# Performance work log

Measured on AMD Instinct MI355X. Metric: run time of the kernel, lower is better.

Reference implementation:

```python
import jax, jax.numpy as jnp
import numpy as np

DIM = 768
NUM_HEADS = 12
HEAD_DIM = DIM // NUM_HEADS
SCALE = HEAD_DIM ** -0.5


def setup_inputs() -> dict:
    key = jax.random.key(0)
    ks = jax.random.split(key, 4)
    x = jax.random.normal(ks[0], (8, 1024, DIM), dtype=jnp.float32)
    # nn.Linear stores weight as [out, in]; we keep that convention.
    w_qkv = jax.random.normal(ks[1], (3 * DIM, DIM), dtype=jnp.float32) * (DIM ** -0.5)
    w_proj = jax.random.normal(ks[2], (DIM, DIM), dtype=jnp.float32) * (DIM ** -0.5)
    b_proj = jax.random.normal(ks[3], (DIM,), dtype=jnp.float32) * 0.02
    return {"x": x, "w_qkv": w_qkv, "w_proj": w_proj, "b_proj": b_proj}


def reference(x, w_qkv, w_proj, b_proj):
    B, N, C = x.shape
    H, D = NUM_HEADS, HEAD_DIM
    # qkv: [B, N, 3C] -> [3, B, H, N, D]
    qkv = jnp.einsum('bnc,oc->bno', x, w_qkv)
    qkv = qkv.reshape(B, N, 3, H, D).transpose(2, 0, 3, 1, 4)
    q, k, v = qkv[0] * SCALE, qkv[1], qkv[2]
    # attention scores [B, H, N, N]
    attn = jnp.einsum('bhnd,bhmd->bhnm', q, k)
    attn = jax.nn.softmax(attn, axis=-1)
    # weighted values -> [B, N, C]
    out = jnp.einsum('bhnm,bhmd->bhnd', attn, v)
    out = out.transpose(0, 2, 1, 3).reshape(B, N, C)
    # output projection
    return jnp.einsum('bnc,oc->bno', out, w_proj) + b_proj
```

## Files before the change

### kernel.cpp

```cpp
#include <hip/hip_runtime.h>
#include <hip/hip_bf16.h>
#include <math.h>


typedef unsigned short u16;
typedef __attribute__((ext_vector_type(8))) short bf16x8;
typedef __attribute__((ext_vector_type(4))) float f32x4;
typedef __attribute__((ext_vector_type(4))) unsigned int u32x4;

#define MFMA_BF16(a, b, c) __builtin_amdgcn_mfma_f32_16x16x32_bf16((a), (b), (c), 0, 0, 0)

static __device__ __forceinline__ void gld_lds16(const void* g, void* l) {
  __builtin_amdgcn_global_load_lds(
      (__attribute__((address_space(1))) void*)(g),
      (__attribute__((address_space(3))) void*)(l), 16, 0, 0);
}

static __device__ __forceinline__ u16 f2bf(float f) {
  __hip_bfloat16 h = __float2bfloat16(f);
  return *(u16*)&h;
}

static __device__ __forceinline__ float fast_exp2(float x) {
#if __has_builtin(__builtin_amdgcn_exp2f)
  return __builtin_amdgcn_exp2f(x);
#else
  return exp2f(x);
#endif
}

static __device__ __forceinline__ void conv4(const float* src, u16* dst, int i) {
  const float4 v = *(const float4*)(src + i);
  float f0 = v.x, f1 = v.y, f2 = v.z, f3 = v.w;
  if (!isfinite(f0)) f0 = 0.f;
  if (!isfinite(f1)) f1 = 0.f;
  if (!isfinite(f2)) f2 = 0.f;
  if (!isfinite(f3)) f3 = 0.f;
  ushort4 o;
  o.x = f2bf(f0); o.y = f2bf(f1); o.z = f2bf(f2); o.w = f2bf(f3);
  *(ushort4*)(dst + i) = o;
}

__global__ __launch_bounds__(256) void convert3_kernel(
    const float* __restrict__ x,  u16* __restrict__ xb,
    const float* __restrict__ wq, u16* __restrict__ wqb,
    const float* __restrict__ wp, u16* __restrict__ wpb)
{
  const int blk = blockIdx.x;
  if (blk < 6144)      conv4(x,  xb,  (blk * 256 + threadIdx.x) * 4);
  else if (blk < 7872) conv4(wq, wqb, ((blk - 6144) * 256 + threadIdx.x) * 4);
  else                 conv4(wp, wpb, ((blk - 7872) * 256 + threadIdx.x) * 4);
}

__device__ __forceinline__ void gemm_tile_768(
    const u16* __restrict__ A, const u16* __restrict__ B,
    int m0, int n0, u16* ldsA, u16* ldsB, f32x4 acc[4][4])
{
  const int tid  = threadIdx.x;
  const int lane = tid & 63;
  const int wave = tid >> 6;
  const int quad = lane >> 4;
  const int l16  = lane & 15;
  const int wm = wave >> 1, wn = wave & 1;

  const u16* gA[4]; const u16* gB[4]; int ldsoff[4];
#pragma unroll
  for (int it = 0; it < 4; ++it) {
    const int c   = it * 256 + tid;
    const int row = c >> 3;
    const int cc  = (c & 7) ^ (row & 7);
    gA[it] = A + (size_t)(m0 + row) * 768 + cc * 8;
    gB[it] = B + (size_t)(n0 + row) * 768 + cc * 8;
    ldsoff[it] = (it * 256 + wave * 64) * 8;
  }

  for (int kt = 0; kt < 12; ++kt) {
    __syncthreads();
#pragma unroll
    for (int it = 0; it < 4; ++it) {
      gld_lds16(gA[it] + kt * 64, ldsA + ldsoff[it]);
      gld_lds16(gB[it] + kt * 64, ldsB + ldsoff[it]);
    }
    __syncthreads();
#pragma unroll
    for (int kc = 0; kc < 2; ++kc) {
      bf16x8 av[4], bv[4];
#pragma unroll
      for (int i = 0; i < 4; ++i) {
        const int rowA = wm * 64 + i * 16 + l16;
        av[i] = *(const bf16x8*)(ldsA + rowA * 64 + (((kc * 4 + quad) ^ (rowA & 7)) * 8));
        const int rowB = wn * 64 + i * 16 + l16;
        bv[i] = *(const bf16x8*)(ldsB + rowB * 64 + (((kc * 4 + quad) ^ (rowB & 7)) * 8));
      }
#pragma unroll
      for (int i = 0; i < 4; ++i)
#pragma unroll
        for (int j = 0; j < 4; ++j)
          acc[i][j] = MFMA_BF16(av[i], bv[j], acc[i][j]);
    }
  }
}


__global__ __launch_bounds__(256, 4) void qkv_gemm_kernel(
    const u16* __restrict__ X, const u16* __restrict__ W,
    u16* __restrict__ Qb, u16* __restrict__ Kb, u16* __restrict__ Vt)
{
  __shared__ alignas(16) u16 lds[2 * 128 * 64];
  u16* ldsA = lds;
  u16* ldsB = lds + 128 * 64;

  const int id0 = blockIdx.y * 18 + blockIdx.x;
  const int swz = (id0 & 7) * 144 + (id0 >> 3);
  const int bx  = swz % 18, by = swz / 18;
  const int n0 = bx * 128;
  const int m0 = by * 128;
  f32x4 acc[4][4];
  const f32x4 zero = {0.f, 0.f, 0.f, 0.f};
#pragma unroll
  for (int i = 0; i < 4; ++i)
#pragma unroll
    for (int j = 0; j < 4; ++j) acc[i][j] = zero;

  gemm_tile_768(X, W, m0, n0, ldsA, ldsB, acc);

  const int tid = threadIdx.x, lane = tid & 63, wave = tid >> 6;
  const int quad = lane >> 4, l16 = lane & 15;
  const int wm = wave >> 1, wn = wave & 1;

  const int which = bx / 6;
  const bool isV = (which == 2);
  const float sc = (which == 0) ? 0.180336880f : 1.0f;
  u16* ep = lds;

  __syncthreads();
#pragma unroll
  for (int i = 0; i < 4; ++i)
#pragma unroll
    for (int j = 0; j < 4; ++j)
#pragma unroll
      for (int r = 0; r < 4; ++r) {
        const int m_l = wm * 64 + i * 16 + quad * 4 + r;
        const int o_l = wn * 64 + j * 16 + l16;
        const int row = isV ? o_l : m_l;
        const int col = isV ? m_l : o_l;
        const int ch  = col >> 3;
        const int chs = (ch & 8) | ((ch & 7) ^ (row & 7));
        ep[row * 128 + chs * 8 + (col & 7)] = f2bf(acc[i][j][r] * sc);
      }
  __syncthreads();

  const int row  = tid >> 1, half = tid & 1;
  const int b_   = m0 >> 10;
  const int nb   = m0 & 1023;
  const int oc0  = n0 - which * 768;
  u16* dst;
  if (!isV) {
    const int h = (oc0 >> 6) + half;
    dst = (which == 0 ? Qb : Kb) + (((size_t)(b_ * 12 + h)) * 1024 + nb + row) * 64;
  } else {
    const int h = (oc0 >> 6) + (row >> 6);
    const int d = row & 63;
    dst = Vt + (((size_t)(b_ * 12 + h)) * 64 + d) * 1024 + nb + half * 64;
  }
#pragma unroll
  for (int c = 0; c < 8; ++c) {
    const int chs = half * 8 + (c ^ (row & 7));
    *(u32x4*)(dst + c * 8) = *(const u32x4*)(ep + row * 128 + chs * 8);
  }
}

__global__ __launch_bounds__(256, 4) void proj_gemm_kernel(
    const u16* __restrict__ A, const u16* __restrict__ W,
    const float* __restrict__ bias, float* __restrict__ out)
{
  __shared__ alignas(16) u16 lds[2 * 128 * 64];
  u16* ldsA = lds;
  u16* ldsB = lds + 128 * 64;

  const int id0 = blockIdx.y * 6 + blockIdx.x;
  const int swz = (id0 & 7) * 48 + (id0 >> 3);
  const int bx  = swz % 6, by = swz / 6;
  const int n0 = bx * 128;
  const int m0 = by * 128;

  f32x4 acc[4][4];
  const f32x4 zero = {0.f, 0.f, 0.f, 0.f};
#pragma unroll
  for (int i = 0; i < 4; ++i)
#pragma unroll
    for (int j = 0; j < 4; ++j) acc[i][j] = zero;

  gemm_tile_768(A, W, m0, n0, ldsA, ldsB, acc);

  const int tid = threadIdx.x, lane = tid & 63, wave = tid >> 6;
  const int quad = lane >> 4, l16 = lane & 15;
  const int wm = wave >> 1, wn = wave & 1;

  float bv4[4];
#pragma unroll
  for (int j = 0; j < 4; ++j) bv4[j] = bias[n0 + wn * 64 + j * 16 + l16];

#pragma unroll
  for (int i = 0; i < 4; ++i)
#pragma unroll
    for (int j = 0; j < 4; ++j)
#pragma unroll
      for (int r = 0; r < 4; ++r) {
        const int m = m0 + wm * 64 + i * 16 + quad * 4 + r;
        out[(size_t)m * 768 + n0 + wn * 64 + j * 16 + l16] = acc[i][j][r] + bv4[j];
      }
}

__global__ __launch_bounds__(256, 3) void attn_kernel(
    const u16* __restrict__ Q, const u16* __restrict__ K,
    const u16* __restrict__ Vt, __hip_bfloat16* __restrict__ O)
{
  __shared__ alignas(16) u16 ldsK[2 * 64 * 64];
  __shared__ alignas(16) u16 ldsV[2 * 64 * 64];
  __shared__ alignas(16) u16 pbuf[4 * 32 * 72];
  const int bh = blockIdx.x;
  const int qb = blockIdx.y;
  const int tid = threadIdx.x;
  const int wave = tid >> 6, lane = tid & 63;
  const int quad = lane >> 4, l16 = lane & 15;
  u16* pw = pbuf + wave * (32 * 72);

  const int q0 = qb * 128 + wave * 32;
  const u16* Kbh = K  + (size_t)bh * (1024 * 64);
  const u16* Vbh = Vt + (size_t)bh * (64 * 1024);

  const u16* gK[2]; const u16* gV[2]; int loK[2], loV[2];
#pragma unroll
  for (int it = 0; it < 2; ++it) {
    const int c = it * 256 + tid;
    {
      const int row = c >> 3, cc = (c & 7) ^ (row & 7);
      gK[it] = Kbh + (size_t)row * 64 + cc * 8;
      loK[it] = (it * 256 + wave * 64) * 8;
    }
    {
      const int row = c >> 3, cc = (c & 7) ^ (row & 7);
      gV[it] = Vbh + (size_t)row * 1024 + cc * 8;
      loV[it] = (it * 256 + wave * 64) * 8;
    }
  }

  bf16x8 aQ0[2], aQ1[2];
#pragma unroll
  for (int s = 0; s < 2; ++s) {
    const u16* qp = Q + ((size_t)bh * 1024 + q0 + s * 16 + l16) * 64 + quad * 8;
    aQ0[s] = *(const bf16x8*)qp;
    aQ1[s] = *(const bf16x8*)(qp + 32);
  }

  f32x4 oacc[2][4];
  const f32x4 zero = {0.f, 0.f, 0.f, 0.f};
#pragma unroll
  for (int s = 0; s < 2; ++s)
#pragma unroll
    for (int db = 0; db < 4; ++db) oacc[s][db] = zero;
  float lacc[2] = {0.f, 0.f};

#pragma unroll
  for (int it = 0; it < 2; ++it) {
    gld_lds16(gK[it], ldsK + loK[it]);
    gld_lds16(gV[it], ldsV + loV[it]);
  }

#pragma unroll 2
  for (int kt = 0; kt < 16; ++kt) {
    const int cur = (kt & 1) * 4096;
    asm volatile("s_waitcnt vmcnt(0)" ::: "memory");
    __builtin_amdgcn_sched_barrier(0);
    __builtin_amdgcn_s_barrier();
    __builtin_amdgcn_sched_barrier(0);
    if (kt < 15) {
      const int nxt = ((kt + 1) & 1) * 4096;
#pragma unroll
      for (int it = 0; it < 2; ++it) {
        gld_lds16(gK[it] + (size_t)(kt + 1) * (64 * 64), ldsK + nxt + loK[it]);
        gld_lds16(gV[it] + (kt + 1) * 64, ldsV + nxt + loV[it]);
      }
    }

    bf16x8 kb0[4], kb1[4];
#pragma unroll
    for (int t = 0; t < 4; ++t) {
      const int row = t * 16 + l16;
      kb0[t] = *(const bf16x8*)(ldsK + cur + row * 64 + (((0 * 4 + quad) ^ (row & 7)) * 8));
      kb1[t] = *(const bf16x8*)(ldsK + cur + row * 64 + (((1 * 4 + quad) ^ (row & 7)) * 8));
    }
    asm volatile("" ::: "memory");
#pragma unroll
    for (int s = 0; s < 2; ++s) {
#pragma unroll
      for (int t = 0; t < 4; ++t) {
        f32x4 z = zero;
        z = MFMA_BF16(kb0[t], aQ0[s], z);
        z = MFMA_BF16(kb1[t], aQ1[s], z);
        const float p0 = fast_exp2(z[0]);
        const float p1 = fast_exp2(z[1]);
        const float p2 = fast_exp2(z[2]);
        const float p3 = fast_exp2(z[3]);
        lacc[s] += (p0 + p1) + (p2 + p3);
        ushort4 pk;
        pk.x = f2bf(p0); pk.y = f2bf(p1); pk.z = f2bf(p2); pk.w = f2bf(p3);
        *(ushort4*)(pw + (s * 16 + l16) * 72 + t * 16 + quad * 4) = pk;
      }
    }
    asm volatile("" ::: "memory");
    bf16x8 pa0[2], pa1[2];
#pragma unroll
    for (int s = 0; s < 2; ++s) {
      const u16* pb = pw + (s * 16 + l16) * 72 + quad * 8;
      pa0[s] = *(const bf16x8*)pb;
      pa1[s] = *(const bf16x8*)(pb + 32);
    }
#pragma unroll
    for (int db = 0; db < 4; ++db) {
      const int d = db * 16 + l16;
      const bf16x8 v0 = *(const bf16x8*)(ldsV + cur + d * 64 + (((0 * 4 + quad) ^ (d & 7))) * 8);
      const bf16x8 v1 = *(const bf16x8*)(ldsV + cur + d * 64 + (((1 * 4 + quad) ^ (d & 7))) * 8);
#pragma unroll
      for (int s = 0; s < 2; ++s) {
        oacc[s][db] = MFMA_BF16(pa0[s], v0, oacc[s][db]);
        oacc[s][db] = MFMA_BF16(pa1[s], v1, oacc[s][db]);
      }
    }
  }

  const int b = bh / 12, h = bh - (bh / 12) * 12;
  float linv[2];
#pragma unroll
  for (int s = 0; s < 2; ++s) {
    float l = lacc[s];
    l += __shfl_xor(l, 16);
    l += __shfl_xor(l, 32);
    linv[s] = 1.f / l;
  }
#pragma unroll
  for (int s = 0; s < 2; ++s) {
#pragma unroll
    for (int r = 0; r < 4; ++r) {
      const float inv = __shfl(linv[s], quad * 4 + r);
      const int n = q0 + s * 16 + quad * 4 + r;
      __hip_bfloat16* orow = O + ((size_t)b * 1024 + n) * 768 + h * 64;
#pragma unroll
      for (int db = 0; db < 4; ++db)
        orow[db * 16 + l16] = __float2bfloat16(oacc[s][db][r] * inv);
    }
  }
}

extern "C" void kernel_launch(void* const* d_in, const int* in_sizes, int n_in,
                              void* d_out, int out_size, void* d_ws, size_t ws_size,
                              hipStream_t stream) {
  const float* x      = (const float*)d_in[0];
  const float* w_qkv  = (const float*)d_in[1];
  const float* w_proj = (const float*)d_in[2];
  const float* b_proj = (const float*)d_in[3];
  float* out = (float*)d_out;

  char* ws = (char*)d_ws;
  const size_t SEG = (size_t)96 * 1024 * 64 * sizeof(u16);
  u16* xb   = (u16*)(ws + 0 * SEG);
  u16* Qb   = (u16*)(ws + 1 * SEG);
  u16* Kb   = (u16*)(ws + 2 * SEG);
  u16* AO   = (u16*)(ws + 3 * SEG);
  u16* Vt   = (u16*)(ws + 4 * SEG);
  u16* wqb  = (u16*)(ws + 5 * SEG);
  u16* wpb  = (u16*)(ws + 5 * SEG + 3538944);

  convert3_kernel<<<8448, 256, 0, stream>>>(x, xb, w_qkv, wqb, w_proj, wpb);
  qkv_gemm_kernel<<<dim3(18, 64), 256, 0, stream>>>(xb, wqb, Qb, Kb, Vt);
  attn_kernel    <<<dim3(96, 8), 256, 0, stream>>>(Qb, Kb, Vt, (__hip_bfloat16*)AO);
  proj_gemm_kernel<<<dim3(6, 64), 256, 0, stream>>>(AO, wpb, b_proj, out);
}
```

Baseline: 184.7 us.

## Double-buffer GEMM K-tiles with smaller K-step to overlap loads and MFMA

Restructures the shared GEMM tile loop from 12 single-buffered K=64 steps into 24 double-buffered K=32 steps. The next tile is prefetched into the other LDS buffer while MFMAs run on the current one, and each step needs one barrier instead of two. The aim is to hide global-to-LDS load latency behind compute. The cost is twice as many iterations and barriers, and a waitcnt of vmcnt(0) that may still serialize part of the work.

New measurement: 190.6 us. +3.2%, slower.

```diff
diff --git a/kernel.cpp b/kernel.cpp
--- a/kernel.cpp
+++ b/kernel.cpp
@@ -63,41 +63,52 @@
   const int l16  = lane & 15;
   const int wm = wave >> 1, wn = wave & 1;
 
-  const u16* gA[4]; const u16* gB[4]; int ldsoff[4];
-#pragma unroll
-  for (int it = 0; it < 4; ++it) {
+  const u16* gA[2]; const u16* gB[2]; int ldso[2];
+#pragma unroll
+  for (int it = 0; it < 2; ++it) {
     const int c   = it * 256 + tid;
-    const int row = c >> 3;
-    const int cc  = (c & 7) ^ (row & 7);
+    const int row = c >> 2;
+    const int cc  = (c & 3) ^ (row & 3);
     gA[it] = A + (size_t)(m0 + row) * 768 + cc * 8;
     gB[it] = B + (size_t)(n0 + row) * 768 + cc * 8;
-    ldsoff[it] = (it * 256 + wave * 64) * 8;
-  }
-
-  for (int kt = 0; kt < 12; ++kt) {
-    __syncthreads();
-#pragma unroll
-    for (int it = 0; it < 4; ++it) {
-      gld_lds16(gA[it] + kt * 64, ldsA + ldsoff[it]);
-      gld_lds16(gB[it] + kt * 64, ldsB + ldsoff[it]);
-    }
-    __syncthreads();
-#pragma unroll
-    for (int kc = 0; kc < 2; ++kc) {
-      bf16x8 av[4], bv[4];
-#pragma unroll
-      for (int i = 0; i < 4; ++i) {
-        const int rowA = wm * 64 + i * 16 + l16;
-        av[i] = *(const bf16x8*)(ldsA + rowA * 64 + (((kc * 4 + quad) ^ (rowA & 7)) * 8));
-        const int rowB = wn * 64 + i * 16 + l16;
-        bv[i] = *(const bf16x8*)(ldsB + rowB * 64 + (((kc * 4 + quad) ^ (rowB & 7)) * 8));
-      }
-#pragma unroll
-      for (int i = 0; i < 4; ++i)
-#pragma unroll
-        for (int j = 0; j < 4; ++j)
-          acc[i][j] = MFMA_BF16(av[i], bv[j], acc[i][j]);
-    }
+    ldso[it] = (it * 256 + wave * 64) * 8;
+  }
+
+#pragma unroll
+  for (int it = 0; it < 2; ++it) {
+    gld_lds16(gA[it], ldsA + ldso[it]);
+    gld_lds16(gB[it], ldsB + ldso[it]);
+  }
+
+#pragma unroll 2
+  for (int kt = 0; kt < 24; ++kt) {
+    const int cur = (kt & 1) * 4096;
+    asm volatile("s_waitcnt vmcnt(0)" ::: "memory");
+    __builtin_amdgcn_sched_barrier(0);
+    __builtin_amdgcn_s_barrier();
+    __builtin_amdgcn_sched_barrier(0);
+    if (kt < 23) {
+      const int nxt = ((kt + 1) & 1) * 4096;
+#pragma unroll
+      for (int it = 0; it < 2; ++it) {
+        gld_lds16(gA[it] + (kt + 1) * 32, ldsA + nxt + ldso[it]);
+        gld_lds16(gB[it] + (kt + 1) * 32, ldsB + nxt + ldso[it]);
+      }
+    }
+
+    bf16x8 av[4], bv[4];
+#pragma unroll
+    for (int i = 0; i < 4; ++i) {
+      const int rowA = wm * 64 + i * 16 + l16;
+      av[i] = *(const bf16x8*)(ldsA + cur + rowA * 32 + ((quad ^ (rowA & 3)) * 8));
+      const int rowB = wn * 64 + i * 16 + l16;
+      bv[i] = *(const bf16x8*)(ldsB + cur + rowB * 32 + ((quad ^ (rowB & 3)) * 8));
+    }
+#pragma unroll
+    for (int i = 0; i < 4; ++i)
+#pragma unroll
+      for (int j = 0; j < 4; ++j)
+        acc[i][j] = MFMA_BF16(av[i], bv[j], acc[i][j]);
   }
 }
 
@@ -108,7 +119,7 @@
 {
   __shared__ alignas(16) u16 lds[2 * 128 * 64];
   u16* ldsA = lds;
-  u16* ldsB = lds + 128 * 64;
+  u16* ldsB = lds + 2 * 128 * 32;
 
   const int id0 = blockIdx.y * 18 + blockIdx.x;
   const int swz = (id0 & 7) * 144 + (id0 >> 3);
@@ -176,7 +187,7 @@
 {
   __shared__ alignas(16) u16 lds[2 * 128 * 64];
   u16* ldsA = lds;
-  u16* ldsB = lds + 128 * 64;
+  u16* ldsB = lds + 2 * 128 * 32;
 
   const int id0 = blockIdx.y * 6 + blockIdx.x;
   const int swz = (id0 & 7) * 48 + (id0 >> 3);
```
